# Optimization experiments

Measured on AMD Instinct MI355X. Metric: run time of the kernel, lower is better.

Reference implementation:

```python
import jax, jax.numpy as jnp
import numpy as np

D = 512
H = 8
DH = D // H
FF = 2 * D
EPS = 1e-5


def _layernorm(x, g, b):
    mu = jnp.mean(x, axis=-1, keepdims=True)
    var = jnp.mean(jnp.square(x - mu), axis=-1, keepdims=True)
    return (x - mu) * jax.lax.rsqrt(var + EPS) * g + b


def setup_inputs() -> dict:
    key = jax.random.key(0)
    ks = jax.random.split(key, 8)
    s = 0.02
    x = jax.random.normal(ks[0], (1, 4096, D), dtype=jnp.float32)
    w_qkv = jax.random.normal(ks[1], (D, 3 * D), dtype=jnp.float32) * s
    b_qkv = jnp.zeros((3 * D,), jnp.float32)
    w_out = jax.random.normal(ks[2], (D, D), dtype=jnp.float32) * s
    b_out = jnp.zeros((D,), jnp.float32)
    w_ff1 = jax.random.normal(ks[3], (D, FF), dtype=jnp.float32) * s
    b_ff1 = jnp.zeros((FF,), jnp.float32)
    w_ff2 = jax.random.normal(ks[4], (FF, D), dtype=jnp.float32) * s
    b_ff2 = jnp.zeros((D,), jnp.float32)
    g1 = jnp.ones((D,), jnp.float32)
    bt1 = jnp.zeros((D,), jnp.float32)
    g2 = jnp.ones((D,), jnp.float32)
    bt2 = jnp.zeros((D,), jnp.float32)
    return {"x": x, "w_qkv": w_qkv, "b_qkv": b_qkv, "w_out": w_out, "b_out": b_out,
            "w_ff1": w_ff1, "b_ff1": b_ff1, "w_ff2": w_ff2, "b_ff2": b_ff2,
            "g1": g1, "bt1": bt1, "g2": g2, "bt2": bt2}


def reference(x, w_qkv, b_qkv, w_out, b_out, w_ff1, b_ff1, w_ff2, b_ff2, g1, bt1, g2, bt2):
    B, S, _ = x.shape
    h = _layernorm(x, g1, bt1)
    qkv = h @ w_qkv + b_qkv                      # [B,S,3D]
    qkv = qkv.reshape(B, S, 3, H, DH)
    q, k, v = qkv[:, :, 0], qkv[:, :, 1], qkv[:, :, 2]   # [B,S,H,DH]
    scores = jnp.einsum('bqhd,bkhd->bhqk', q, k) / np.sqrt(DH).astype(np.float32)
    causal = jnp.tril(jnp.ones((S, S), dtype=bool))
    scores = jnp.where(causal, scores, -jnp.inf)
    attn = jax.nn.softmax(scores, axis=-1)
    out = jnp.einsum('bhqk,bkhd->bqhd', attn, v).reshape(B, S, D)
    x = x + out @ w_out + b_out
    h2 = _layernorm(x, g2, bt2)
    ff = jax.nn.gelu(h2 @ w_ff1 + b_ff1, approximate=False) @ w_ff2 + b_ff2
    return x + ff
```

## Files before the change

kernel.cpp:

```cpp
#include <hip/hip_runtime.h>
#include <math.h>

#define D 512
#define H 8
#define DH 64
#define S 4096
#define FF 1024

typedef __attribute__((ext_vector_type(8))) short bf16x8;
typedef __attribute__((ext_vector_type(4))) float f32x4;
typedef __attribute__((ext_vector_type(16))) float f32x16;

__device__ __forceinline__ unsigned short f2bf(float f) {
    union { float f; unsigned u; } c; c.f = f;
    unsigned r = (c.u + 0x7fff + ((c.u >> 16) & 1)) >> 16;
    return (unsigned short)r;
}
__device__ __forceinline__ float bf2f(unsigned short u) {
    union { unsigned u; float f; } c; c.u = ((unsigned)u) << 16;
    return c.f;
}

__device__ __forceinline__ void gl_lds16(const void* g, void* l) {
    __builtin_amdgcn_global_load_lds(
        (const __attribute__((address_space(1))) void*)g,
        (__attribute__((address_space(3))) void*)l, 16, 0, 0);
}

__global__ __launch_bounds__(256) void prep_kernel(const float* __restrict__ wqkv,
                                                   const float* __restrict__ wout,
                                                   const float* __restrict__ wff1,
                                                   const float* __restrict__ wff2,
                                                   unsigned short* __restrict__ oqkv,
                                                   unsigned short* __restrict__ oout,
                                                   unsigned short* __restrict__ off1,
                                                   unsigned short* __restrict__ off2,
                                                   const float* __restrict__ x,
                                                   const float* __restrict__ g1,
                                                   const float* __restrict__ bt1,
                                                   unsigned short* __restrict__ hout) {
    __shared__ unsigned short tile[32][33];
    __shared__ float red[8];
    int id = blockIdx.x;
    int tid = threadIdx.x;
    if (id >= 2048) {
        int row = id - 2048;
        const float* xr = x + (size_t)row * D;
        float2 v = *(const float2*)(xr + tid * 2);
        float s = v.x + v.y;
        float sq = v.x * v.x + v.y * v.y;
#pragma unroll
        for (int m = 1; m < 64; m <<= 1) { s += __shfl_xor(s, m); sq += __shfl_xor(sq, m); }
        int wave = tid >> 6, lane = tid & 63;
        if (lane == 0) { red[wave] = s; red[4 + wave] = sq; }
        __syncthreads();
        s = red[0] + red[1] + red[2] + red[3];
        sq = red[4] + red[5] + red[6] + red[7];
        float mu = s * (1.f / D);
        float var = sq * (1.f / D) - mu * mu;
        float rstd = rsqrtf(var + 1e-5f);
        int i = tid * 2;
        float2 gg = *(const float2*)(g1 + i);
        float2 bb = *(const float2*)(bt1 + i);
        hout[(size_t)row * D + i]     = f2bf((v.x - mu) * rstd * gg.x + bb.x);
        hout[(size_t)row * D + i + 1] = f2bf((v.y - mu) * rstd * gg.y + bb.y);
        return;
    }
    const float* src; unsigned short* dst; int K, N, lid;
    if (id < 768)       { src = wqkv; dst = oqkv; K = 512;  N = 1536; lid = id; }
    else if (id < 1024) { src = wout; dst = oout; K = 512;  N = 512;  lid = id - 768; }
    else if (id < 1536) { src = wff1; dst = off1; K = 512;  N = 1024; lid = id - 1024; }
    else                { src = wff2; dst = off2; K = 1024; N = 512;  lid = id - 1536; }
    int nb = N / 32;
    int n0 = (lid % nb) * 32, k0 = (lid / nb) * 32;
    int tx = tid & 31, ty = tid >> 5;
#pragma unroll
    for (int i = 0; i < 32; i += 8)
        tile[ty + i][tx] = f2bf(src[(size_t)(k0 + ty + i) * N + n0 + tx]);
    __syncthreads();
#pragma unroll
    for (int i = 0; i < 32; i += 8)
        dst[(size_t)(n0 + ty + i) * K + k0 + tx] = tile[tx][ty + i];
}

__global__ __launch_bounds__(256) void ln_kernel(const float* __restrict__ x,
                                                 const float* __restrict__ g,
                                                 const float* __restrict__ bta,
                                                 unsigned short* __restrict__ out) {
    int row = blockIdx.x, tid = threadIdx.x;
    const float* xr = x + (size_t)row * D;
    float2 v = *(const float2*)(xr + tid * 2);
    float s = v.x + v.y;
    float sq = v.x * v.x + v.y * v.y;
#pragma unroll
    for (int m = 1; m < 64; m <<= 1) { s += __shfl_xor(s, m); sq += __shfl_xor(sq, m); }
    __shared__ float red[8];
    int wave = tid >> 6, lane = tid & 63;
    if (lane == 0) { red[wave] = s; red[4 + wave] = sq; }
    __syncthreads();
    s = red[0] + red[1] + red[2] + red[3];
    sq = red[4] + red[5] + red[6] + red[7];
    float mu = s * (1.f / D);
    float var = sq * (1.f / D) - mu * mu;
    float rstd = rsqrtf(var + 1e-5f);
    int i = tid * 2;
    float2 gg = *(const float2*)(g + i);
    float2 bb = *(const float2*)(bta + i);
    out[(size_t)row * D + i]     = f2bf((v.x - mu) * rstd * gg.x + bb.x);
    out[(size_t)row * D + i + 1] = f2bf((v.y - mu) * rstd * gg.y + bb.y);
}

enum { EPI_BF16 = 0, EPI_RESID_F32 = 1, EPI_GELU_BF16 = 2 };

template <int EPI, int WMI, int BNT, bool QKV>
__global__ __launch_bounds__(256, WMI == 4 ? 2 : (WMI == 2 ? 3 : 4))
void gemm5_kernel(const unsigned short* __restrict__ A,
                  const unsigned short* __restrict__ BT,
                  const float* __restrict__ bias,
                  const float* __restrict__ resid,
                  void* __restrict__ out,
                  unsigned short* __restrict__ vTout,
                  int M, int N, int K) {
    constexpr int BM = 32 * WMI;
    constexpr int APH = BM / 32;
    constexpr int BPH = BNT / 32;
    constexpr int NLD = APH + BPH;
    constexpr int NI = BNT / 32;
    __shared__ __align__(16) unsigned short sA[2][BM * 64];
    __shared__ __align__(16) unsigned short sB[2][BNT * 64];

    int tid = threadIdx.x;
    int wave = tid >> 6, lane = tid & 63;
    int quad = lane >> 4, l16 = lane & 15;
    int lx = l16 & 7;
    int wr = (wave >> 1) * (BM / 2), wc = (wave & 1) * (BNT / 2);
    int m0 = blockIdx.y * BM, n0 = blockIdx.x * BNT;

    f32x4 acc[WMI][NI];
#pragma unroll
    for (int i = 0; i < WMI; i++)
#pragma unroll
        for (int j = 0; j < NI; j++) acc[i][j] = (f32x4){0.f, 0.f, 0.f, 0.f};

    int srow = tid >> 3;
    int spc = tid & 7;
    int scc = spc ^ (srow & 7);
    const unsigned short* Abase = A + (size_t)(m0 + srow) * K + scc * 8;
    const unsigned short* Bbase = BT + (size_t)(n0 + srow) * K + scc * 8;
    int wofs = (tid & ~63) * 8;

    auto stage = [&](int k0, int buf) {
#pragma unroll
        for (int ph = 0; ph < APH; ph++)
            gl_lds16(Abase + (size_t)(ph * 32) * K + k0, sA[buf] + wofs + ph * 2048);
#pragma unroll
        for (int ph = 0; ph < BPH; ph++)
            gl_lds16(Bbase + (size_t)(ph * 32) * K + k0, sB[buf] + wofs + ph * 2048);
    };

    int nk = K / 64;
    stage(0, 0);
    for (int ki = 0; ki < nk; ki++) {
        int buf = ki & 1;
        if (ki + 1 < nk) {
            stage((ki + 1) * 64, buf ^ 1);
            if constexpr (NLD == 3)
                asm volatile("s_waitcnt vmcnt(3)" ::: "memory");
            else if constexpr (NLD == 4)
                asm volatile("s_waitcnt vmcnt(4)" ::: "memory");
            else if constexpr (NLD == 6)
                asm volatile("s_waitcnt vmcnt(6)" ::: "memory");
            else
                asm volatile("s_waitcnt vmcnt(8)" ::: "memory");
        } else {
            asm volatile("s_waitcnt vmcnt(0)" ::: "memory");
        }
        __syncthreads();

#pragma unroll
        for (int ks = 0; ks < 2; ks++) {
            int cxs = ((ks * 4 + quad) ^ lx) * 8;
            bf16x8 af[WMI], bfr[NI];
#pragma unroll
            for (int mi = 0; mi < WMI; mi++)
                af[mi] = *(const bf16x8*)(&sA[buf][(wr + mi * 16 + l16) * 64 + cxs]);
#pragma unroll
            for (int ni = 0; ni < NI; ni++)
                bfr[ni] = *(const bf16x8*)(&sB[buf][(wc + ni * 16 + l16) * 64 + cxs]);
#pragma unroll
            for (int mi = 0; mi < WMI; mi++)
#pragma unroll
                for (int ni = 0; ni < NI; ni++)
                    acc[mi][ni] = __builtin_amdgcn_mfma_f32_16x16x32_bf16(af[mi], bfr[ni], acc[mi][ni], 0, 0, 0);
        }
        __syncthreads();
    }

#pragma unroll
    for (int mi = 0; mi < WMI; mi++)
#pragma unroll
        for (int ni = 0; ni < NI; ni++) {
            int col = n0 + wc + ni * 16 + l16;
            float bs = bias[col];
            int row0 = m0 + wr + mi * 16 + quad * 4;
            unsigned short tv[4];
#pragma unroll
            for (int r = 0; r < 4; r++) {
                float v = acc[mi][ni][r] + bs;
                size_t idx = (size_t)(row0 + r) * N + col;
                if constexpr (EPI == EPI_RESID_F32) {
                    ((float*)out)[idx] = v + resid[idx];
                } else if constexpr (EPI == EPI_GELU_BF16) {
                    v = 0.5f * v * (1.f + erff(v * 0.70710678118f));
                    ((unsigned short*)out)[idx] = f2bf(v);
                } else {
                    unsigned short b = f2bf(v);
                    ((unsigned short*)out)[idx] = b;
                    tv[r] = b;
                }
            }
            if constexpr (QKV) {
                if (col >= 2 * D) {
                    unsigned lo = (unsigned)tv[0] | ((unsigned)tv[1] << 16);
                    unsigned hi = (unsigned)tv[2] | ((unsigned)tv[3] << 16);
                    uint2 pk; pk.x = lo; pk.y = hi;
                    *(uint2*)(vTout + (size_t)(col - 2 * D) * S + row0) = pk;
                }
            }
        }
}

#define LDO 68

__global__ __launch_bounds__(256, 4) void flash8_kernel(const unsigned short* __restrict__ qkv,
                                                        const unsigned short* __restrict__ vT,
                                                        unsigned short* __restrict__ O_part,
                                                        float* __restrict__ l_part) {
    __shared__ __align__(16) unsigned short sMem[4][64 * 64];

    int tid = threadIdx.x;
    int w = tid >> 6, lane = tid & 63;
    int lq = lane & 31, hb = lane >> 5;

    int h = blockIdx.x & 7;
    int u = blockIdx.x >> 3;
    int Q = 31, c = 0, acc = 0;
    for (int qq = 31; qq >= 0; --qq) {
        int n = (qq >> 2) + 1;
        if (u < acc + n) { Q = qq; c = u - acc; break; }
        acc += n;
    }
    int T = 2 * Q + 2;
    int t0c = c * 8;
    int t1c = min(t0c + 8, T);
    int q0w = Q * 128 + w * 32;
    int qrow = q0w + lq;
    int qmax = q0w + 31;

    const float CEXP = 0.18033688f;

    bf16x8 qf[4];
#pragma unroll
    for (int dc = 0; dc < 4; dc++)
        qf[dc] = *(const bf16x8*)(qkv + (size_t)qrow * (3 * D) + h * DH + dc * 16 + hb * 8);

    f32x16 oa[2];
#pragma unroll
    for (int i = 0; i < 16; i++) { oa[0][i] = 0.f; oa[1][i] = 0.f; }
    float l4[4] = {0.f, 0.f, 0.f, 0.f};

    int rr = tid >> 3;
    int spc = tid & 7;
    int scc = spc ^ (rr & 7);
    const unsigned short* kgb = qkv + (size_t)rr * (3 * D) + D + h * DH + scc * 8;
    const unsigned short* vgb = vT + (size_t)(h * DH + rr) * S + scc * 8;

    auto stage = [&](int t, int buf) {
        const unsigned short* kg = kgb + (size_t)t * 64 * (3 * D);
        const unsigned short* vg = vgb + t * 64;
        unsigned short* dK = sMem[buf] + w * 512;
        unsigned short* dV = sMem[2 + buf] + w * 512;
        gl_lds16(kg, dK);
        gl_lds16(kg + (size_t)32 * (3 * D), dK + 2048);
        gl_lds16(vg, dV);
        gl_lds16(vg + (size_t)32 * S, dV + 2048);
    };

    stage(t0c, 0);
    for (int t = t0c; t < t1c; ++t) {
        int buf = (t - t0c) & 1;
        asm volatile("s_waitcnt vmcnt(0)" ::: "memory");
        __syncthreads();
        if (t + 1 < t1c) stage(t + 1, buf ^ 1);

        if (64 * t > qmax) continue;

        f32x16 sa[2];
#pragma unroll
        for (int i = 0; i < 16; i++) { sa[0][i] = 0.f; sa[1][i] = 0.f; }
#pragma unroll
        for (int kt = 0; kt < 2; kt++)
#pragma unroll
            for (int dc = 0; dc < 4; dc++) {
                int ch = ((dc * 2 + hb) ^ (lq & 7)) * 8;
                bf16x8 kfr = *(const bf16x8*)(&sMem[buf][(kt * 32 + lq) * 64 + ch]);
                sa[kt] = __builtin_amdgcn_mfma_f32_32x32x16_bf16(kfr, qf[dc], sa[kt], 0, 0, 0);
            }

        bool dmask = (64 * t + 63 > qmax);
        unsigned p2[2][8];
        if (!dmask) {
#pragma unroll
            for (int kt = 0; kt < 2; kt++) {
                float e[16];
#pragma unroll
                for (int r = 0; r < 16; r++) {
                    e[r] = __builtin_amdgcn_exp2f(sa[kt][r] * CEXP);
                    l4[r & 3] += e[r];
                }
#pragma unroll
                for (int p = 0; p < 8; p++)
                    p2[kt][p] = ((unsigned)f2bf(e[2 * p + 1]) << 16) | f2bf(e[2 * p]);
            }
        } else {
#pragma unroll
            for (int kt = 0; kt < 2; kt++) {
                float e[16];
#pragma unroll
                for (int r = 0; r < 16; r++) {
                    float v = __builtin_amdgcn_exp2f(sa[kt][r] * CEXP);
                    int key = 64 * t + kt * 32 + (r & 3) + 8 * (r >> 2) + 4 * hb;
                    if (key > qrow) v = 0.f;
                    e[r] = v;
                    l4[r & 3] += v;
                }
#pragma unroll
                for (int p = 0; p < 8; p++)
                    p2[kt][p] = ((unsigned)f2bf(e[2 * p + 1]) << 16) | f2bf(e[2 * p]);
            }
        }

#pragma unroll
        for (int kc = 0; kc < 4; kc++) {
            int kt = kc >> 1;
            int b0i = (kc & 1) * 4;
            unsigned a0 = p2[kt][b0i + 0], a1 = p2[kt][b0i + 1];
            unsigned b0 = p2[kt][b0i + 2], b1 = p2[kt][b0i + 3];
            unsigned s0 = hb ? a0 : b0, s1 = hb ? a1 : b1;
            unsigned x0 = __shfl_xor(s0, 32), x1 = __shfl_xor(s1, 32);
            unsigned l0 = hb ? b0 : a0, l1 = hb ? b1 : a1;
            union { unsigned u[4]; bf16x8 v; } fr;
            fr.u[0] = hb ? x0 : l0;
            fr.u[1] = hb ? x1 : l1;
            fr.u[2] = hb ? l0 : x0;
            fr.u[3] = hb ? l1 : x1;
#pragma unroll
            for (int dt = 0; dt < 2; dt++) {
                int ch = ((kc * 2 + hb) ^ (lq & 7)) * 8;
                bf16x8 vfr = *(const bf16x8*)(&sMem[2 + buf][(dt * 32 + lq) * 64 + ch]);
                oa[dt] = __builtin_amdgcn_mfma_f32_32x32x16_bf16(vfr, fr.v, oa[dt], 0, 0, 0);
            }
        }
    }

    float lsum = (l4[0] + l4[1]) + (l4[2] + l4[3]);
    lsum += __shfl_xor(lsum, 32);
    if (hb == 0)
        l_part[((size_t)c * H + h) * S + q0w + lq] = lsum;

    __syncthreads();
    unsigned short* sOw = (unsigned short*)sMem + w * 32 * LDO;
#pragma unroll
    for (int kt = 0; kt < 2; kt++)
#pragma unroll
        for (int r = 0; r < 16; r++) {
            int d = kt * 32 + (r & 3) + 8 * (r >> 2) + 4 * hb;
            sOw[lq * LDO + d] = f2bf(oa[kt][r]);
        }
    asm volatile("s_waitcnt lgkmcnt(0)" ::: "memory");
    unsigned short* Op = O_part + ((size_t)c * S + q0w) * D + h * DH;
#pragma unroll
    for (int it = 0; it < 4; it++) {
        int rq = (lane >> 3) + it * 8;
        bf16x8 val = *(const bf16x8*)(sOw + rq * LDO + (lane & 7) * 8);
        *(bf16x8*)(Op + (size_t)rq * D + (lane & 7) * 8) = val;
    }
}

__global__ __launch_bounds__(256) void norm_kernel(const unsigned short* __restrict__ O_part,
                                                   const float* __restrict__ l_part,
                                                   unsigned short* __restrict__ O) {
    int idx = blockIdx.x * 256 + threadIdx.x;
    int row = idx >> 6;
    int c8 = (idx & 63) * 8;
    int h = c8 >> 6;
    int nch = ((row >> 7) >> 2) + 1;
    float o[8] = {0.f, 0.f, 0.f, 0.f, 0.f, 0.f, 0.f, 0.f};
    float l = 0.f;
    for (int cc = 0; cc < nch; cc++) {
        bf16x8 v = *(const bf16x8*)(O_part + ((size_t)cc * S + row) * D + c8);
#pragma unroll
        for (int j = 0; j < 8; j++) o[j] += bf2f((unsigned short)v[j]);
        l += l_part[((size_t)cc * H + h) * S + row];
    }
    float inv = 1.f / l;
    bf16x8 r;
#pragma unroll
    for (int j = 0; j < 8; j++) r[j] = (short)f2bf(o[j] * inv);
    *(bf16x8*)(O + (size_t)row * D + c8) = r;
}

extern "C" void kernel_launch(void* const* d_in, const int* in_sizes, int n_in,
                              void* d_out, int out_size, void* d_ws, size_t ws_size,
                              hipStream_t stream) {
    const float* x     = (const float*)d_in[0];
    const float* w_qkv = (const float*)d_in[1];
    const float* b_qkv = (const float*)d_in[2];
    const float* w_out = (const float*)d_in[3];
    const float* b_out = (const float*)d_in[4];
    const float* w_ff1 = (const float*)d_in[5];
    const float* b_ff1 = (const float*)d_in[6];
    const float* w_ff2 = (const float*)d_in[7];
    const float* b_ff2 = (const float*)d_in[8];
    const float* g1    = (const float*)d_in[9];
    const float* bt1   = (const float*)d_in[10];
    const float* g2    = (const float*)d_in[11];
    const float* bt2   = (const float*)d_in[12];

    char* ws = (char*)d_ws;
    size_t off = 0;
    auto alloc = [&](size_t bytes) {
        void* p = ws + off;
        off += (bytes + 255) & ~(size_t)255;
        return p;
    };
    unsigned short* hbuf   = (unsigned short*)alloc((size_t)S * D * 2);
    unsigned short* qkvbuf = (unsigned short*)alloc((size_t)S * 3 * D * 2);
    unsigned short* vTbuf  = (unsigned short*)alloc((size_t)D * S * 2);
    unsigned short* Obuf   = (unsigned short*)alloc((size_t)S * D * 2);
    unsigned short* wqkvT  = (unsigned short*)alloc((size_t)3 * D * D * 2);
    unsigned short* woutT  = (unsigned short*)alloc((size_t)D * D * 2);
    unsigned short* wff1T  = (unsigned short*)alloc((size_t)FF * D * 2);
    unsigned short* wff2T  = (unsigned short*)alloc((size_t)D * FF * 2);
    unsigned short* Opart  = (unsigned short*)alloc((size_t)8 * S * D * 2);
    float*          lpart  = (float*)alloc((size_t)8 * H * S * 4);
    unsigned short* h2buf  = hbuf;
    unsigned short* ff1buf = qkvbuf;
    float*          x2buf  = (float*)Opart;

    prep_kernel<<<dim3(2048 + S), 256, 0, stream>>>(w_qkv, w_out, w_ff1, w_ff2,
                                                    wqkvT, woutT, wff1T, wff2T,
                                                    x, g1, bt1, hbuf);
    gemm5_kernel<EPI_BF16, 2, 128, true><<<dim3(12, 64), 256, 0, stream>>>(
        hbuf, wqkvT, b_qkv, nullptr, qkvbuf, vTbuf, S, 3 * D, D);
    flash8_kernel<<<dim3(1152), 256, 0, stream>>>(qkvbuf, vTbuf, Opart, lpart);
    norm_kernel<<<dim3(S * D / 8 / 256), 256, 0, stream>>>(Opart, lpart, Obuf);
    gemm5_kernel<EPI_RESID_F32, 1, 64, false><<<dim3(8, 128), 256, 0, stream>>>(
        Obuf, woutT, b_out, x, x2buf, nullptr, S, D, D);
    ln_kernel<<<S, 256, 0, stream>>>(x2buf, g2, bt2, h2buf);
    gemm5_kernel<EPI_GELU_BF16, 1, 64, false><<<dim3(16, 128), 256, 0, stream>>>(
        h2buf, wff1T, b_ff1, nullptr, ff1buf, nullptr, S, FF, D);
    gemm5_kernel<EPI_RESID_F32, 1, 64, false><<<dim3(8, 128), 256, 0, stream>>>(
        ff1buf, wff2T, b_ff2, x2buf, (float*)d_out, nullptr, S, D, FF);
}
```

Before: 187.4 us.

## Add double-buffered 32x64 GEMM kernel for out-proj and FFN GEMMs

Introduces a new GEMM kernel with 32x64 output tiles, a K-step of 128, XOR-swizzled LDS and double-buffered global-to-LDS loads that overlap the next tile's fetch with the current MFMA work. It replaces the older gemm5 kernel for the output projection and both FFN GEMMs, keeping the same grid sizes. The aim is to hide memory latency and raise MFMA throughput in these GEMMs, at the cost of more LDS per block and lower occupancy (launch bounds 3 instead of 4).

```diff
diff --git a/kernel.cpp b/kernel.cpp
--- a/kernel.cpp
+++ b/kernel.cpp
@@ -230,6 +230,89 @@
         }
 }
 
+template <int EPI>
+__global__ __launch_bounds__(256, 3)
+void gemm6_kernel(const unsigned short* __restrict__ A,
+                  const unsigned short* __restrict__ BT,
+                  const float* __restrict__ bias,
+                  const float* __restrict__ resid,
+                  void* __restrict__ out,
+                  int M, int N, int K) {
+    __shared__ __align__(16) unsigned short sA[2][32 * 128];
+    __shared__ __align__(16) unsigned short sB[2][64 * 128];
+
+    int tid = threadIdx.x;
+    int wave = tid >> 6, lane = tid & 63;
+    int quad = lane >> 4, l16 = lane & 15;
+    int wr = (wave >> 1) * 16, wc = (wave & 1) * 32;
+    int m0 = blockIdx.y * 32, n0 = blockIdx.x * 64;
+
+    f32x4 acc[2];
+    acc[0] = (f32x4){0.f, 0.f, 0.f, 0.f};
+    acc[1] = (f32x4){0.f, 0.f, 0.f, 0.f};
+
+    int srow = tid >> 4;
+    int spc = tid & 15;
+    int scc = spc ^ srow;
+    const unsigned short* Abase = A + (size_t)(m0 + srow) * K + scc * 8;
+    const unsigned short* Bbase = BT + (size_t)(n0 + srow) * K + scc * 8;
+    int wofs = (tid & ~63) * 8;
+
+    auto stage = [&](int k0, int buf) {
+#pragma unroll
+        for (int ph = 0; ph < 2; ph++)
+            gl_lds16(Abase + (size_t)(ph * 16) * K + k0, sA[buf] + wofs + ph * 2048);
+#pragma unroll
+        for (int ph = 0; ph < 4; ph++)
+            gl_lds16(Bbase + (size_t)(ph * 16) * K + k0, sB[buf] + wofs + ph * 2048);
+    };
+
+    int nk = K / 128;
+    stage(0, 0);
+    for (int ki = 0; ki < nk; ki++) {
+        int buf = ki & 1;
+        if (ki + 1 < nk) {
+            stage((ki + 1) * 128, buf ^ 1);
+            asm volatile("s_waitcnt vmcnt(6)" ::: "memory");
+        } else {
+            asm volatile("s_waitcnt vmcnt(0)" ::: "memory");
+        }
+        __syncthreads();
+
+#pragma unroll
+        for (int ks = 0; ks < 4; ks++) {
+            int cxs = ((ks * 4 + quad) ^ l16) * 8;
+            bf16x8 af = *(const bf16x8*)(&sA[buf][(wr + l16) * 128 + cxs]);
+#pragma unroll
+            for (int ni = 0; ni < 2; ni++) {
+                bf16x8 bfr = *(const bf16x8*)(&sB[buf][(wc + ni * 16 + l16) * 128 + cxs]);
+                acc[ni] = __builtin_amdgcn_mfma_f32_16x16x32_bf16(af, bfr, acc[ni], 0, 0, 0);
+            }
+        }
+        __syncthreads();
+    }
+
+#pragma unroll
+    for (int ni = 0; ni < 2; ni++) {
+        int col = n0 + wc + ni * 16 + l16;
+        float bs = bias[col];
+        int row0 = m0 + wr + quad * 4;
+#pragma unroll
+        for (int r = 0; r < 4; r++) {
+            float v = acc[ni][r] + bs;
+            size_t idx = (size_t)(row0 + r) * N + col;
+            if constexpr (EPI == EPI_RESID_F32) {
+                ((float*)out)[idx] = v + resid[idx];
+            } else if constexpr (EPI == EPI_GELU_BF16) {
+                v = 0.5f * v * (1.f + erff(v * 0.70710678118f));
+                ((unsigned short*)out)[idx] = f2bf(v);
+            } else {
+                ((unsigned short*)out)[idx] = f2bf(v);
+            }
+        }
+    }
+}
+
 #define LDO 68
 
 __global__ __launch_bounds__(256, 4) void flash8_kernel(const unsigned short* __restrict__ qkv,
@@ -455,11 +538,11 @@
         hbuf, wqkvT, b_qkv, nullptr, qkvbuf, vTbuf, S, 3 * D, D);
     flash8_kernel<<<dim3(1152), 256, 0, stream>>>(qkvbuf, vTbuf, Opart, lpart);
     norm_kernel<<<dim3(S * D / 8 / 256), 256, 0, stream>>>(Opart, lpart, Obuf);
-    gemm5_kernel<EPI_RESID_F32, 1, 64, false><<<dim3(8, 128), 256, 0, stream>>>(
-        Obuf, woutT, b_out, x, x2buf, nullptr, S, D, D);
+    gemm6_kernel<EPI_RESID_F32><<<dim3(8, 128), 256, 0, stream>>>(
+        Obuf, woutT, b_out, x, x2buf, S, D, D);
     ln_kernel<<<S, 256, 0, stream>>>(x2buf, g2, bt2, h2buf);
-    gemm5_kernel<EPI_GELU_BF16, 1, 64, false><<<dim3(16, 128), 256, 0, stream>>>(
-        h2buf, wff1T, b_ff1, nullptr, ff1buf, nullptr, S, FF, D);
-    gemm5_kernel<EPI_RESID_F32, 1, 64, false><<<dim3(8, 128), 256, 0, stream>>>(
-        ff1buf, wff2T, b_ff2, x2buf, (float*)d_out, nullptr, S, D, FF);
-}
+    gemm6_kernel<EPI_GELU_BF16><<<dim3(16, 128), 256, 0, stream>>>(
+        h2buf, wff1T, b_ff1, nullptr, ff1buf, S, FF, D);
+    gemm6_kernel<EPI_RESID_F32><<<dim3(8, 128), 256, 0, stream>>>(
+        ff1buf, wff2T, b_ff2, x2buf, (float*)d_out, S, D, FF);
+}
```

New measurement: 194.8 us. 1.04x slower.
